# Kernel tuning notes

Measured on AMD Instinct MI355X. Metric: run time of the kernel, lower is better.

The kernel has to match this reference:

```python
import jax, jax.numpy as jnp
import numpy as np

B, N, R = 16, 512, 10
DE, DR, DOUT = 256, 64, 256

def setup_inputs() -> dict:
    key = jax.random.key(0)
    k1, k2, k3, k4 = jax.random.split(key, 4)
    node_features = jax.random.normal(k1, (B, N, DE), dtype=jnp.float32)
    relation_features = jax.random.normal(k2, (B, R, DR), dtype=jnp.float32)
    adj = jax.random.uniform(k3, (B, R, N, N), dtype=jnp.float32)
    in_dim = (DE + DR) * R
    bound = float(np.sqrt(6.0 / (in_dim + DOUT)))  # xavier_uniform
    W = jax.random.uniform(k4, (DOUT, in_dim), dtype=jnp.float32, minval=-bound, maxval=bound)
    bias = jnp.zeros((DOUT,), dtype=jnp.float32)
    return {"node_features": node_features, "relation_features": relation_features,
            "adj": adj, "W": W, "bias": bias}

def reference(node_features, relation_features, adj, W, bias):
    # adj: [B,R,N,N]; node_features: [B,N,De]; relation_features: [B,R,Dr]
    # Per relation r: bmm(adj[:,r], cat([node, rel_r broadcast], -1))
    # Node part: adj @ node_features for every relation at once.
    node_part = jnp.einsum('brnm,bmd->brnd', adj, node_features)      # [B,R,N,De]
    # Relation part: adj @ (rel_r repeated over rows) == rowsum(adj) * rel_r
    rel_part = adj.sum(axis=-1)[..., None] * relation_features[:, :, None, :]  # [B,R,N,Dr]
    supports = jnp.concatenate([node_part, rel_part], axis=-1)        # [B,R,N,De+Dr]
    supports = supports.transpose(0, 2, 1, 3).reshape(node_features.shape[0],
                                                      node_features.shape[1], -1)  # [B,N,R*(De+Dr)]
    return supports @ W.T + bias
```

## Files before the change

### kernel.cpp

```cpp
#include <hip/hip_runtime.h>
#include <stdint.h>

#define B_     16
#define N_     512
#define R_     10
#define DE_    256
#define DR_    64
#define DOUT_  256
#define INDIM_ 3200
#define BLK_   320
#define RN_    5120
#define SPLITS_ 4
#define CPS_    20

typedef __bf16          v8bf  __attribute__((ext_vector_type(8)));
typedef unsigned short  v8us  __attribute__((ext_vector_type(8)));
typedef unsigned short  v4us  __attribute__((ext_vector_type(4)));
typedef float           f32x4 __attribute__((ext_vector_type(4)));

static __device__ __forceinline__ unsigned short f2b(float f) {
  union { float f; unsigned u; } c; c.f = f;
  unsigned r = c.u + 0x7FFFu + ((c.u >> 16) & 1u);
  return (unsigned short)(r >> 16);
}

static __device__ __forceinline__ v8bf us2bf(v8us u) {
  union { v8us u; v8bf b; } c; c.u = u; return c.b;
}

static __device__ __forceinline__ void gl_lds16(const void* g, void* l) {
  __builtin_amdgcn_global_load_lds(
      (const __attribute__((address_space(1))) void*)g,
      (__attribute__((address_space(3))) void*)l, 16, 0, 0);
}

__global__ void prep_all(const float* __restrict__ nf, const float* __restrict__ W,
                         const float* __restrict__ rel,
                         unsigned short* __restrict__ nodeB,
                         unsigned short* __restrict__ WnB,
                         float* __restrict__ Uf) {
  const int bb = blockIdx.x;
  const int tid = threadIdx.x;
  if (bb < 256) {
    const size_t base = (size_t)bb * 8192;
#pragma unroll
    for (int p = 0; p < 4; ++p) {
      size_t off = base + (size_t)p * 2048 + (size_t)tid * 8;
      float4 x = *(const float4*)(nf + off);
      float4 y = *(const float4*)(nf + off + 4);
      v8us u;
      u[0] = f2b(x.x); u[1] = f2b(x.y); u[2] = f2b(x.z); u[3] = f2b(x.w);
      u[4] = f2b(y.x); u[5] = f2b(y.y); u[6] = f2b(y.z); u[7] = f2b(y.w);
      *(v8us*)(nodeB + off) = u;
    }
  } else if (bb < 896) {
    int idx = (bb - 256) * 1024 + tid * 4;
    int r = idx >> 16;
    int o = (idx >> 8) & 255;
    int d = idx & 255;
    float4 x = *(const float4*)(W + (size_t)o * INDIM_ + r * BLK_ + d);
    v4us u;
    u[0] = f2b(x.x); u[1] = f2b(x.y); u[2] = f2b(x.z); u[3] = f2b(x.w);
    *(v4us*)(WnB + idx) = u;
  } else {
    int idx = (bb - 896) * 256 + tid;
    int o  = idx & 255;
    int br = idx >> 8;
    int r  = br % R_;
    const float* rp = rel + (size_t)br * DR_;
    const float* wp = W + (size_t)o * INDIM_ + r * BLK_ + DE_;
    float v = 0.f;
#pragma unroll 8
    for (int d = 0; d < DR_; ++d) v += rp[d] * wp[d];
    Uf[idx] = v;
  }
}

__global__ void stageA_gemm(const unsigned short* __restrict__ nodeB,
                            const unsigned short* __restrict__ WnB,
                            const float* __restrict__ Uf,
                            unsigned short* __restrict__ Gp) {
  __shared__ unsigned short S[2 * 16384];
  const int br = blockIdx.x;
  const int b  = br / R_, r = br % R_;
  const int o0 = blockIdx.y * 128;
  const int m0 = blockIdx.z * 128;
  const int tid  = threadIdx.x;
  const int lane = tid & 63;
  const int wave = tid >> 6;
  const int wm = wave >> 1, wn = wave & 1;
  const int quad = lane >> 4, l16 = lane & 15;

  const unsigned short* Wb = WnB + (size_t)r * (DOUT_ * DE_);
  const unsigned short* Nb = nodeB + (size_t)b * (N_ * DE_);

  f32x4 acc[4][4];
#pragma unroll
  for (int i = 0; i < 4; ++i)
#pragma unroll
    for (int j = 0; j < 4; ++j) acc[i][j] = f32x4{0.f, 0.f, 0.f, 0.f};

  const int srl = lane >> 3;
  const int skc = lane & 7;

  {
    unsigned short* Al = S;
    unsigned short* Bl = S + 8192;
#pragma unroll
    for (int it = 0; it < 4; ++it) {
      int rowblk = it * 32 + wave * 8;
      int rl = rowblk + srl;
      int kc = skc ^ (rl & 7);
      gl_lds16(Wb + (size_t)(o0 + rl) * DE_ + kc * 8, Al + rowblk * 64);
      gl_lds16(Nb + (size_t)(m0 + rl) * DE_ + kc * 8, Bl + rowblk * 64);
    }
  }
  __syncthreads();

  for (int t = 0; t < 4; ++t) {
    unsigned short* Sc = S + (t & 1) * 16384;
    unsigned short* Sn = S + ((t & 1) ^ 1) * 16384;
    if (t < 3) {
      const int dk = (t + 1) * 64;
      unsigned short* Aln = Sn;
      unsigned short* Bln = Sn + 8192;
#pragma unroll
      for (int it = 0; it < 4; ++it) {
        int rowblk = it * 32 + wave * 8;
        int rl = rowblk + srl;
        int kc = skc ^ (rl & 7);
        gl_lds16(Wb + (size_t)(o0 + rl) * DE_ + dk + kc * 8, Aln + rowblk * 64);
        gl_lds16(Nb + (size_t)(m0 + rl) * DE_ + dk + kc * 8, Bln + rowblk * 64);
      }
    }
    const unsigned short* Al = Sc;
    const unsigned short* Bl = Sc + 8192;
#pragma unroll
    for (int ks = 0; ks < 2; ++ks) {
      const int kb = ks * 4;
      v8bf av[4], bv[4];
#pragma unroll
      for (int mi = 0; mi < 4; ++mi) {
        int m = wm * 64 + mi * 16 + l16;
        av[mi] = us2bf(*(const v8us*)(Al + m * 64 + (((kb + quad) ^ (m & 7)) * 8)));
      }
#pragma unroll
      for (int ni = 0; ni < 4; ++ni) {
        int c = wn * 64 + ni * 16 + l16;
        bv[ni] = us2bf(*(const v8us*)(Bl + c * 64 + (((kb + quad) ^ (c & 7)) * 8)));
      }
#pragma unroll
      for (int mi = 0; mi < 4; ++mi)
#pragma unroll
        for (int ni = 0; ni < 4; ++ni)
          acc[mi][ni] = __builtin_amdgcn_mfma_f32_16x16x32_bf16(av[mi], bv[ni], acc[mi][ni], 0, 0, 0);
    }
    __syncthreads();
  }

#pragma unroll
  for (int mi = 0; mi < 4; ++mi)
#pragma unroll
    for (int t = 0; t < 4; ++t) {
      int o_loc = wm * 64 + mi * 16 + quad * 4 + t;
      float u = Uf[(size_t)br * DOUT_ + o0 + o_loc];
#pragma unroll
      for (int ni = 0; ni < 4; ++ni) {
        int m_loc = wn * 64 + ni * 16 + l16;
        S[o_loc * 128 + m_loc] = f2b(acc[mi][ni][t] + u);
      }
    }
  __syncthreads();
#pragma unroll
  for (int p = 0; p < 8; ++p) {
    int idx16 = p * 2048 + tid * 8;
    int orow = idx16 >> 7;
    int moff = idx16 & 127;
    unsigned short* dst = Gp + ((size_t)(b * DOUT_ + o0 + orow)) * RN_ + r * N_ + m0 + moff;
    *(v8us*)dst = *(const v8us*)(S + idx16);
  }
}

__global__ __launch_bounds__(256, 2)
void stageB_gemm(const float* __restrict__ adj,
                 const unsigned short* __restrict__ Gp,
                 float* __restrict__ part) {
  __shared__ unsigned short SB[2 * 20480];
  const int b  = blockIdx.x;
  const int n0 = blockIdx.y * 64;
  const int sp = blockIdx.z;
  const int tid  = threadIdx.x;
  const int lane = tid & 63;
  const int wave = tid >> 6;
  const int quad = lane >> 4, l16 = lane & 15;

  const float* Ab = adj + (size_t)b * (R_ * N_ * N_);
  const unsigned short* Gb = Gp + (size_t)b * (DOUT_ * RN_);

  f32x4 acc[4][4];
#pragma unroll
  for (int i = 0; i < 4; ++i)
#pragma unroll
    for (int j = 0; j < 4; ++j) acc[i][j] = f32x4{0.f, 0.f, 0.f, 0.f};

  const int ar   = tid >> 2;
  const int ac16 = tid & 3;
  const int sl0  = (ac16 * 2) ^ (ar & 7);
  const int sl1  = (ac16 * 2 + 1) ^ (ar & 7);
  const int brl = wave * 8 + (lane >> 3);
  const int bkc = lane & 7;

  int c = sp * CPS_;

  {
    const int r = c >> 3, mc = (c & 7) << 6, k0 = c << 6;
    unsigned short* Aln = SB;
    unsigned short* Bln = SB + 4096;
#pragma unroll
    for (int s = 0; s < 8; ++s) {
      int rl = s * 32 + brl;
      int kc = bkc ^ (rl & 7);
      gl_lds16(Gb + (size_t)rl * RN_ + k0 + kc * 8, Bln + (s * 32 + wave * 8) * 64);
    }
    const float* Ap = Ab + ((size_t)r * N_ + n0) * N_ + mc + (size_t)ar * N_ + ac16 * 16;
    float4 a0 = *(const float4*)(Ap);
    float4 a1 = *(const float4*)(Ap + 4);
    float4 a2 = *(const float4*)(Ap + 8);
    float4 a3 = *(const float4*)(Ap + 12);
    v8us u0, u1;
    u0[0] = f2b(a0.x); u0[1] = f2b(a0.y); u0[2] = f2b(a0.z); u0[3] = f2b(a0.w);
    u0[4] = f2b(a1.x); u0[5] = f2b(a1.y); u0[6] = f2b(a1.z); u0[7] = f2b(a1.w);
    u1[0] = f2b(a2.x); u1[1] = f2b(a2.y); u1[2] = f2b(a2.z); u1[3] = f2b(a2.w);
    u1[4] = f2b(a3.x); u1[5] = f2b(a3.y); u1[6] = f2b(a3.z); u1[7] = f2b(a3.w);
    *(v8us*)(Aln + ar * 64 + sl0 * 8) = u0;
    *(v8us*)(Aln + ar * 64 + sl1 * 8) = u1;
  }
  __syncthreads();

  for (int t = 0; t < CPS_; ++t) {
    unsigned short* Sc = SB + (t & 1) * 20480;
    unsigned short* Sn = SB + ((t & 1) ^ 1) * 20480;
    float4 a0, a1, a2, a3;
    const bool pf = (t + 1 < CPS_);
    if (pf) {
      const int c1 = c + 1;
      const int r = c1 >> 3, mc = (c1 & 7) << 6, k0 = c1 << 6;
      unsigned short* Bln = Sn + 4096;
#pragma unroll
      for (int s = 0; s < 8; ++s) {
        int rl = s * 32 + brl;
        int kc = bkc ^ (rl & 7);
        gl_lds16(Gb + (size_t)rl * RN_ + k0 + kc * 8, Bln + (s * 32 + wave * 8) * 64);
      }
      const float* Ap = Ab + ((size_t)r * N_ + n0) * N_ + mc + (size_t)ar * N_ + ac16 * 16;
      a0 = *(const float4*)(Ap);
      a1 = *(const float4*)(Ap + 4);
      a2 = *(const float4*)(Ap + 8);
      a3 = *(const float4*)(Ap + 12);
    }
    const unsigned short* Alc = Sc;
    const unsigned short* Blc = Sc + 4096;
#pragma unroll
    for (int ks = 0; ks < 2; ++ks) {
      const int kb = ks * 4;
      v8bf av[4], bv[4];
#pragma unroll
      for (int mi = 0; mi < 4; ++mi) {
        int m = mi * 16 + l16;
        av[mi] = us2bf(*(const v8us*)(Alc + m * 64 + (((kb + quad) ^ (m & 7)) * 8)));
      }
#pragma unroll
      for (int ni = 0; ni < 4; ++ni) {
        int o = wave * 64 + ni * 16 + l16;
        bv[ni] = us2bf(*(const v8us*)(Blc + o * 64 + (((kb + quad) ^ (o & 7)) * 8)));
      }
#pragma unroll
      for (int mi = 0; mi < 4; ++mi)
#pragma unroll
        for (int ni = 0; ni < 4; ++ni)
          acc[mi][ni] = __builtin_amdgcn_mfma_f32_16x16x32_bf16(av[mi], bv[ni], acc[mi][ni], 0, 0, 0);
    }
    if (pf) {
      v8us u0, u1;
      u0[0] = f2b(a0.x); u0[1] = f2b(a0.y); u0[2] = f2b(a0.z); u0[3] = f2b(a0.w);
      u0[4] = f2b(a1.x); u0[5] = f2b(a1.y); u0[6] = f2b(a1.z); u0[7] = f2b(a1.w);
      u1[0] = f2b(a2.x); u1[1] = f2b(a2.y); u1[2] = f2b(a2.z); u1[3] = f2b(a2.w);
      u1[4] = f2b(a3.x); u1[5] = f2b(a3.y); u1[6] = f2b(a3.z); u1[7] = f2b(a3.w);
      *(v8us*)(Sn + ar * 64 + sl0 * 8) = u0;
      *(v8us*)(Sn + ar * 64 + sl1 * 8) = u1;
    }
    __syncthreads();
    ++c;
  }

  float* pb = part + (((size_t)sp * B_ + b) * N_) * DOUT_;
#pragma unroll
  for (int mi = 0; mi < 4; ++mi)
#pragma unroll
    for (int t4 = 0; t4 < 4; ++t4) {
      int row = n0 + mi * 16 + quad * 4 + t4;
#pragma unroll
      for (int ni = 0; ni < 4; ++ni) {
        int col = wave * 64 + ni * 16 + l16;
        pb[(size_t)row * DOUT_ + col] = acc[mi][ni][t4];
      }
    }
}

__global__ void reduce_out(const float* __restrict__ part, const float* __restrict__ bias,
                           float* __restrict__ out) {
  const size_t idx = (size_t)blockIdx.x * 256 + threadIdx.x;
  const size_t stride = (size_t)B_ * N_ * DOUT_ / 4;
  f32x4 a = *(const f32x4*)(bias + (idx & 63) * 4);
#pragma unroll
  for (int s = 0; s < SPLITS_; ++s) {
    f32x4 p = *(const f32x4*)((const float*)part + (stride * s + idx) * 4);
    a += p;
  }
  *(f32x4*)(out + idx * 4) = a;
}

extern "C" void kernel_launch(void* const* d_in, const int* in_sizes, int n_in,
                              void* d_out, int out_size, void* d_ws, size_t ws_size,
                              hipStream_t stream) {
  const float* node = (const float*)d_in[0];
  const float* rel  = (const float*)d_in[1];
  const float* adj  = (const float*)d_in[2];
  const float* W    = (const float*)d_in[3];
  const float* bias = (const float*)d_in[4];
  float* out = (float*)d_out;

  char* ws = (char*)d_ws;
  unsigned short* nodeB = (unsigned short*)(ws);
  unsigned short* WnB   = (unsigned short*)(ws + ((size_t)5 << 20));
  float*          Uf    = (float*)         (ws + ((size_t)7 << 20));
  unsigned short* Gp    = (unsigned short*)(ws + ((size_t)8 << 20));
  float*          part  = (float*)         (ws + ((size_t)48 << 20));

  prep_all<<<dim3(1056), 256, 0, stream>>>(node, W, rel, nodeB, WnB, Uf);
  stageA_gemm<<<dim3(B_ * R_, DOUT_ / 128, N_ / 128), 256, 0, stream>>>(nodeB, WnB, Uf, Gp);
  stageB_gemm<<<dim3(B_, N_ / 64, SPLITS_), 256, 0, stream>>>(adj, Gp, part);
  reduce_out<<<dim3((B_ * N_ * DOUT_ / 4) / 256), 256, 0, stream>>>(part, bias, out);
}
```

Measured before the change: 295.7 us.

## Enlarge stageB tile to 128 rows with 512 threads and triple-buffered pipeline

New measurement: 300.5 us. No clear change (+1.6%).

```diff
diff --git a/kernel.cpp b/kernel.cpp
--- a/kernel.cpp
+++ b/kernel.cpp
@@ -33,6 +33,12 @@
       (const __attribute__((address_space(1))) void*)g,
       (__attribute__((address_space(3))) void*)l, 16, 0, 0);
 }
+
+static __device__ __forceinline__ void waitv12() { asm volatile("s_waitcnt vmcnt(12)" ::: "memory"); }
+static __device__ __forceinline__ void waitv8()  { asm volatile("s_waitcnt vmcnt(8)"  ::: "memory"); }
+static __device__ __forceinline__ void waitv0()  { asm volatile("s_waitcnt vmcnt(0)"  ::: "memory"); }
+static __device__ __forceinline__ void waitl0()  { asm volatile("s_waitcnt lgkmcnt(0)" ::: "memory"); }
+#define SCHED0() __builtin_amdgcn_sched_barrier(0)
 
 __global__ void prep_all(const float* __restrict__ nf, const float* __restrict__ W,
                          const float* __restrict__ rel,
@@ -181,17 +187,21 @@
   }
 }
 
-__global__ __launch_bounds__(256, 2)
+__global__ __launch_bounds__(512, 1)
 void stageB_gemm(const float* __restrict__ adj,
                  const unsigned short* __restrict__ Gp,
                  float* __restrict__ part) {
-  __shared__ unsigned short SB[2 * 20480];
+  __shared__ unsigned short SB[65536];
+  unsigned short* Bring = SB;
+  unsigned short* Aring = SB + 49152;
   const int b  = blockIdx.x;
-  const int n0 = blockIdx.y * 64;
+  const int n0 = blockIdx.y * 128;
   const int sp = blockIdx.z;
   const int tid  = threadIdx.x;
   const int lane = tid & 63;
   const int wave = tid >> 6;
+  const int wm = wave >> 2;
+  const int wn = wave & 3;
   const int quad = lane >> 4, l16 = lane & 15;
 
   const float* Ab = adj + (size_t)b * (R_ * N_ * N_);
@@ -203,105 +213,114 @@
 #pragma unroll
     for (int j = 0; j < 4; ++j) acc[i][j] = f32x4{0.f, 0.f, 0.f, 0.f};
 
-  const int ar   = tid >> 2;
-  const int ac16 = tid & 3;
-  const int sl0  = (ac16 * 2) ^ (ar & 7);
-  const int sl1  = (ac16 * 2 + 1) ^ (ar & 7);
+  const int ar0 = tid >> 3;
+  const int ac8 = tid & 7;
+  const int acs = ac8 ^ (ar0 & 7);
   const int brl = wave * 8 + (lane >> 3);
   const int bkc = lane & 7;
-
-  int c = sp * CPS_;
-
-  {
-    const int r = c >> 3, mc = (c & 7) << 6, k0 = c << 6;
-    unsigned short* Aln = SB;
-    unsigned short* Bln = SB + 4096;
-#pragma unroll
-    for (int s = 0; s < 8; ++s) {
-      int rl = s * 32 + brl;
-      int kc = bkc ^ (rl & 7);
-      gl_lds16(Gb + (size_t)rl * RN_ + k0 + kc * 8, Bln + (s * 32 + wave * 8) * 64);
-    }
-    const float* Ap = Ab + ((size_t)r * N_ + n0) * N_ + mc + (size_t)ar * N_ + ac16 * 16;
-    float4 a0 = *(const float4*)(Ap);
-    float4 a1 = *(const float4*)(Ap + 4);
-    float4 a2 = *(const float4*)(Ap + 8);
-    float4 a3 = *(const float4*)(Ap + 12);
-    v8us u0, u1;
-    u0[0] = f2b(a0.x); u0[1] = f2b(a0.y); u0[2] = f2b(a0.z); u0[3] = f2b(a0.w);
-    u0[4] = f2b(a1.x); u0[5] = f2b(a1.y); u0[6] = f2b(a1.z); u0[7] = f2b(a1.w);
-    u1[0] = f2b(a2.x); u1[1] = f2b(a2.y); u1[2] = f2b(a2.z); u1[3] = f2b(a2.w);
-    u1[4] = f2b(a3.x); u1[5] = f2b(a3.y); u1[6] = f2b(a3.z); u1[7] = f2b(a3.w);
-    *(v8us*)(Aln + ar * 64 + sl0 * 8) = u0;
-    *(v8us*)(Aln + ar * 64 + sl1 * 8) = u1;
-  }
-  __syncthreads();
-
+  const int c0 = sp * CPS_;
+
+  float4 As[3][4];
+
+#define ISSUE_B(slot, cc) do { \
+    unsigned short* Bd = Bring + (slot) * 16384; \
+    const int k0b = (cc) << 6; \
+    _Pragma("unroll") \
+    for (int s = 0; s < 4; ++s) { \
+      int rl = s * 64 + brl; \
+      int kc = bkc ^ (rl & 7); \
+      gl_lds16(Gb + (size_t)rl * RN_ + k0b + kc * 8, Bd + (s * 64 + wave * 8) * 64); \
+    } } while (0)
+
+#define ISSUE_A(set, cc) do { \
+    const float* g = Ab + ((size_t)((cc) >> 3) * N_ + n0) * N_ + ((cc) & 7) * 64 \
+                     + (size_t)ar0 * N_ + ac8 * 8; \
+    As[set][0] = *(const float4*)(g); \
+    As[set][1] = *(const float4*)(g + 4); \
+    As[set][2] = *(const float4*)(g + 64 * N_); \
+    As[set][3] = *(const float4*)(g + 64 * N_ + 4); } while (0)
+
+#define CONV_A(set, abuf) do { \
+    v8us u0, u1; \
+    u0[0] = f2b(As[set][0].x); u0[1] = f2b(As[set][0].y); \
+    u0[2] = f2b(As[set][0].z); u0[3] = f2b(As[set][0].w); \
+    u0[4] = f2b(As[set][1].x); u0[5] = f2b(As[set][1].y); \
+    u0[6] = f2b(As[set][1].z); u0[7] = f2b(As[set][1].w); \
+    u1[0] = f2b(As[set][2].x); u1[1] = f2b(As[set][2].y); \
+    u1[2] = f2b(As[set][2].z); u1[3] = f2b(As[set][2].w); \
+    u1[4] = f2b(As[set][3].x); u1[5] = f2b(As[set][3].y); \
+    u1[6] = f2b(As[set][3].z); u1[7] = f2b(As[set][3].w); \
+    unsigned short* Ad = Aring + (abuf) * 8192; \
+    *(v8us*)(Ad + ar0 * 64 + acs * 8) = u0; \
+    *(v8us*)(Ad + (ar0 + 64) * 64 + acs * 8) = u1; } while (0)
+
+#define COMPUTE(bslot, abuf) do { \
+    const unsigned short* Alc = Aring + (abuf) * 8192; \
+    const unsigned short* Blc = Bring + (bslot) * 16384; \
+    _Pragma("unroll") \
+    for (int ks = 0; ks < 2; ++ks) { \
+      const int kb = ks * 4; \
+      v8bf av[4], bv[4]; \
+      _Pragma("unroll") \
+      for (int mi = 0; mi < 4; ++mi) { \
+        int m = wm * 64 + mi * 16 + l16; \
+        av[mi] = us2bf(*(const v8us*)(Alc + m * 64 + (((kb + quad) ^ (m & 7)) * 8))); \
+      } \
+      _Pragma("unroll") \
+      for (int ni = 0; ni < 4; ++ni) { \
+        int o = wn * 64 + ni * 16 + l16; \
+        bv[ni] = us2bf(*(const v8us*)(Blc + o * 64 + (((kb + quad) ^ (o & 7)) * 8))); \
+      } \
+      _Pragma("unroll") \
+      for (int mi = 0; mi < 4; ++mi) \
+        _Pragma("unroll") \
+        for (int ni = 0; ni < 4; ++ni) \
+          acc[mi][ni] = __builtin_amdgcn_mfma_f32_16x16x32_bf16(av[mi], bv[ni], acc[mi][ni], 0, 0, 0); \
+    } } while (0)
+
+  ISSUE_B(0, c0 + 0); SCHED0();
+  ISSUE_A(0, c0 + 0); SCHED0();
+  ISSUE_B(1, c0 + 1); SCHED0();
+  ISSUE_A(1, c0 + 1); SCHED0();
+  ISSUE_A(2, c0 + 2); SCHED0();
+  waitv12();
+  SCHED0();
+  CONV_A(0, 0);
+  waitl0();
+
+#pragma unroll
   for (int t = 0; t < CPS_; ++t) {
-    unsigned short* Sc = SB + (t & 1) * 20480;
-    unsigned short* Sn = SB + ((t & 1) ^ 1) * 20480;
-    float4 a0, a1, a2, a3;
-    const bool pf = (t + 1 < CPS_);
-    if (pf) {
-      const int c1 = c + 1;
-      const int r = c1 >> 3, mc = (c1 & 7) << 6, k0 = c1 << 6;
-      unsigned short* Bln = Sn + 4096;
-#pragma unroll
-      for (int s = 0; s < 8; ++s) {
-        int rl = s * 32 + brl;
-        int kc = bkc ^ (rl & 7);
-        gl_lds16(Gb + (size_t)rl * RN_ + k0 + kc * 8, Bln + (s * 32 + wave * 8) * 64);
-      }
-      const float* Ap = Ab + ((size_t)r * N_ + n0) * N_ + mc + (size_t)ar * N_ + ac16 * 16;
-      a0 = *(const float4*)(Ap);
-      a1 = *(const float4*)(Ap + 4);
-      a2 = *(const float4*)(Ap + 8);
-      a3 = *(const float4*)(Ap + 12);
-    }
-    const unsigned short* Alc = Sc;
-    const unsigned short* Blc = Sc + 4096;
-#pragma unroll
-    for (int ks = 0; ks < 2; ++ks) {
-      const int kb = ks * 4;
-      v8bf av[4], bv[4];
-#pragma unroll
-      for (int mi = 0; mi < 4; ++mi) {
-        int m = mi * 16 + l16;
-        av[mi] = us2bf(*(const v8us*)(Alc + m * 64 + (((kb + quad) ^ (m & 7)) * 8)));
-      }
+    __builtin_amdgcn_s_barrier();
+    SCHED0();
+    if (t + 2 < CPS_) { ISSUE_B((t + 2) % 3, c0 + t + 2); }
+    SCHED0();
+    if (t + 3 < CPS_) { ISSUE_A((t + 3) % 3, c0 + t + 3); }
+    SCHED0();
+    COMPUTE(t % 3, t & 1);
+    if (t + 1 < CPS_) {
+      if (t < 17)       waitv12();
+      else if (t == 17) waitv8();
+      else              waitv0();
+      SCHED0();
+      CONV_A((t + 1) % 3, (t + 1) & 1);
+    }
+    waitl0();
+  }
+
+#undef ISSUE_B
+#undef ISSUE_A
+#undef CONV_A
+#undef COMPUTE
+
+  float* pb = part + (((size_t)sp * B_ + b) * N_) * DOUT_;
+#pragma unroll
+  for (int mi = 0; mi < 4; ++mi)
+#pragma unroll
+    for (int t4 = 0; t4 < 4; ++t4) {
+      int row = n0 + wm * 64 + mi * 16 + quad * 4 + t4;
 #pragma unroll
       for (int ni = 0; ni < 4; ++ni) {
-        int o = wave * 64 + ni * 16 + l16;
-        bv[ni] = us2bf(*(const v8us*)(Blc + o * 64 + (((kb + quad) ^ (o & 7)) * 8)));
-      }
-#pragma unroll
-      for (int mi = 0; mi < 4; ++mi)
-#pragma unroll
-        for (int ni = 0; ni < 4; ++ni)
-          acc[mi][ni] = __builtin_amdgcn_mfma_f32_16x16x32_bf16(av[mi], bv[ni], acc[mi][ni], 0, 0, 0);
-    }
-    if (pf) {
-      v8us u0, u1;
-      u0[0] = f2b(a0.x); u0[1] = f2b(a0.y); u0[2] = f2b(a0.z); u0[3] = f2b(a0.w);
-      u0[4] = f2b(a1.x); u0[5] = f2b(a1.y); u0[6] = f2b(a1.z); u0[7] = f2b(a1.w);
-      u1[0] = f2b(a2.x); u1[1] = f2b(a2.y); u1[2] = f2b(a2.z); u1[3] = f2b(a2.w);
-      u1[4] = f2b(a3.x); u1[5] = f2b(a3.y); u1[6] = f2b(a3.z); u1[7] = f2b(a3.w);
-      *(v8us*)(Sn + ar * 64 + sl0 * 8) = u0;
-      *(v8us*)(Sn + ar * 64 + sl1 * 8) = u1;
-    }
-    __syncthreads();
-    ++c;
-  }
-
-  float* pb = part + (((size_t)sp * B_ + b) * N_) * DOUT_;
-#pragma unroll
-  for (int mi = 0; mi < 4; ++mi)
-#pragma unroll
-    for (int t4 = 0; t4 < 4; ++t4) {
-      int row = n0 + mi * 16 + quad * 4 + t4;
-#pragma unroll
-      for (int ni = 0; ni < 4; ++ni) {
-        int col = wave * 64 + ni * 16 + l16;
+        int col = wn * 64 + ni * 16 + l16;
         pb[(size_t)row * DOUT_ + col] = acc[mi][ni][t4];
       }
     }
@@ -339,6 +358,6 @@
 
   prep_all<<<dim3(1056), 256, 0, stream>>>(node, W, rel, nodeB, WnB, Uf);
   stageA_gemm<<<dim3(B_ * R_, DOUT_ / 128, N_ / 128), 256, 0, stream>>>(nodeB, WnB, Uf, Gp);
-  stageB_gemm<<<dim3(B_, N_ / 64, SPLITS_), 256, 0, stream>>>(adj, Gp, part);
+  stageB_gemm<<<dim3(B_, N_ / 128, SPLITS_), 512, 0, stream>>>(adj, Gp, part);
   reduce_out<<<dim3((B_ * N_ * DOUT_ / 4) / 256), 256, 0, stream>>>(part, bias, out);
 }
```
